# Kernel tuning notes

Hardware: AMD Instinct MI355X
Metric: run time of the kernel (lower is better)

The kernel has to match this reference:

```python
import jax, jax.numpy as jnp
import numpy as np

DIM = 768
H = 12          # num_heads
KV = 4          # kv_heads
D = DIM // H    # head_dim = 64
ROPE_BASE = 10000.0
WINDOW = 8
B, N = 4, 1024


def setup_inputs() -> dict:
    key = jax.random.key(0)
    ks = jax.random.split(key, 8)
    s = 0.02  # weight scale for sane magnitudes
    return {
        "x": jax.random.normal(ks[0], (B, N, DIM), jnp.float32),
        "Wq": jax.random.normal(ks[1], (2 * DIM, DIM), jnp.float32) * s,
        "Wk": jax.random.normal(ks[2], (2 * DIM * KV // H, DIM), jnp.float32) * s,
        "Wv1": jax.random.normal(ks[3], (DIM * KV // H, DIM), jnp.float32) * s,
        "Wv2": jax.random.normal(ks[4], (DIM * KV // H, DIM), jnp.float32) * s,
        "lambda_p": jnp.full((H, 1, 1), -2.0, jnp.float32),
        "Wo": jax.random.normal(ks[5], (DIM, DIM), jnp.float32) * s,
        "bo": jax.random.normal(ks[6], (DIM,), jnp.float32) * s,
    }


def _rotate_half(x):
    x1 = x[..., ::2]
    x2 = x[..., 1::2]
    return jnp.stack([-x2, x1], axis=-1).reshape(x.shape)


def _rope_cos_sin(n, dtype):
    side = int(n ** 0.5)
    if side * side == n:
        h = np.arange(side, dtype=np.float32)
        gh, gw = np.meshgrid(h, h, indexing="ij")
        pos_h, pos_w = gh.reshape(-1), gw.reshape(-1)
    else:
        pos_h = np.arange(n, dtype=np.float32)
        pos_w = np.zeros_like(pos_h)
    dim_half = D // 2
    inv_freq = ROPE_BASE ** (-np.arange(dim_half, dtype=np.float32) / dim_half)
    theta = np.concatenate([pos_h[:, None] * inv_freq[None, :],
                            pos_w[:, None] * inv_freq[None, :]], axis=1)  # [N, D]
    cos = jnp.asarray(np.cos(theta), dtype)[None, None]  # [1,1,N,D]
    sin = jnp.asarray(np.sin(theta), dtype)[None, None]
    return cos, sin


def _apply_rope(q, cos, sin):
    return q * cos + _rotate_half(q) * sin


def _qk_norm(t):
    return t / (jnp.linalg.norm(t, axis=-1, keepdims=True) + 1e-6)


def _window_mask(n, dtype):
    side = int(n ** 0.5)
    if side * side == n:
        h = np.arange(side)
        gh, gw = np.meshgrid(h, h, indexing="ij")
        coords = np.stack([gh.reshape(-1), gw.reshape(-1)], axis=1)  # [N,2]
        dist = np.abs(coords[:, None, :] - coords[None, :, :]).max(-1)  # Chebyshev
    else:
        idx = np.arange(n)
        dist = np.abs(idx[None, :] - idx[:, None])
    return jnp.asarray(np.where(dist > WINDOW, -np.inf, 0.0).astype(np.float32), dtype)


def _attend(q, k, v, mask):
    # q,k,v: [B,H,N,D]; mask additive [N,N]
    scale = 1.0 / np.sqrt(D)
    scores = jnp.einsum("bhnd,bhmd->bhnm", q, k) * scale + mask
    return jnp.einsum("bhnm,bhmd->bhnd", jax.nn.softmax(scores, axis=-1), v)


def reference(x, Wq, Wk, Wv1, Wv2, lambda_p, Wo, bo):
    b, n, c = x.shape
    rep = H // KV
    q = (x @ Wq.T).reshape(b, n, 2, H, D).transpose(2, 0, 3, 1, 4)   # [2,B,H,N,D]
    k = (x @ Wk.T).reshape(b, n, 2, KV, D).transpose(2, 0, 3, 1, 4)  # [2,B,KV,N,D]
    v1 = (x @ Wv1.T).reshape(b, n, KV, D).transpose(0, 2, 1, 3)      # [B,KV,N,D]
    v2 = (x @ Wv2.T).reshape(b, n, KV, D).transpose(0, 2, 1, 3)
    q1, q2 = q[0], q[1]
    k1, k2 = k[0], k[1]
    # GQA: repeat_interleave over head axis
    k1 = jnp.repeat(k1, rep, axis=1)
    k2 = jnp.repeat(k2, rep, axis=1)
    v1 = jnp.repeat(v1, rep, axis=1)
    v2 = jnp.repeat(v2, rep, axis=1)
    cos, sin = _rope_cos_sin(n, x.dtype)
    q1, q2 = _apply_rope(q1, cos, sin), _apply_rope(q2, cos, sin)
    k1, k2 = _apply_rope(k1, cos, sin), _apply_rope(k2, cos, sin)
    q1, q2, k1, k2 = _qk_norm(q1), _qk_norm(q2), _qk_norm(k1), _qk_norm(k2)
    mask = _window_mask(n, x.dtype)
    out1 = _attend(q1, k1, v1, mask)
    out2 = _attend(q2, k2, v2, mask)
    lam = jax.nn.softplus(lambda_p)  # [H,1,1] broadcasts over [B,H,N,D]
    out = out1 - lam[None] * out2
    out = out.transpose(0, 2, 1, 3).reshape(b, n, c)
    return out @ Wo.T + bo
```

## Files before the change

### kernel.cpp

```cpp
#include <hip/hip_runtime.h>
#include <hip/hip_bf16.h>

#define BATCH 4
#define NSEQ  1024
#define DIM   768
#define NH    12
#define NKV   4
#define HD    64
#define NTOK  (BATCH*NSEQ)

using bf16 = __hip_bfloat16;
typedef __attribute__((ext_vector_type(8))) short short8;
typedef __attribute__((ext_vector_type(4))) float floatx4;

__device__ __forceinline__ float b2f(short x) {
  unsigned u = ((unsigned)(unsigned short)x) << 16;
  return __builtin_bit_cast(float, u);
}
__device__ __forceinline__ unsigned short f2b(float f) {
  unsigned u = __builtin_bit_cast(unsigned, f);
  unsigned r = u + 0x7FFF + ((u >> 16) & 1);
  return (unsigned short)(r >> 16);
}

__device__ __forceinline__ void load_lds_16(const bf16* g, bf16* l) {
  __builtin_amdgcn_global_load_lds(
      (const __attribute__((address_space(1))) void*)g,
      (__attribute__((address_space(3))) void*)l, 16, 0, 0);
}

__global__ __launch_bounds__(256) void cvt_all(
    const float* __restrict__ x,  const float* __restrict__ wq,
    const float* __restrict__ wk, const float* __restrict__ wv1,
    const float* __restrict__ wv2, const float* __restrict__ wo,
    bf16* __restrict__ xb,  bf16* __restrict__ wqb, bf16* __restrict__ wkb,
    bf16* __restrict__ wv1b, bf16* __restrict__ wv2b, bf16* __restrict__ wob)
{
  int i = blockIdx.x * 256 + threadIdx.x;
  const float* s; bf16* d; int off;
  if      (i <  786432) { s = x;   d = xb;   off = i; }
  else if (i < 1081344) { s = wq;  d = wqb;  off = i -  786432; }
  else if (i < 1179648) { s = wk;  d = wkb;  off = i - 1081344; }
  else if (i < 1228800) { s = wv1; d = wv1b; off = i - 1179648; }
  else if (i < 1277952) { s = wv2; d = wv2b; off = i - 1228800; }
  else                  { s = wo;  d = wob;  off = i - 1277952; }
  float4 f = reinterpret_cast<const float4*>(s)[off];
  ushort4 u;
  u.x = f2b(f.x); u.y = f2b(f.y); u.z = f2b(f.z); u.w = f2b(f.w);
  reinterpret_cast<ushort4*>(d)[off] = u;
}

__global__ __launch_bounds__(256, 2) void gemm_qkv(
    const bf16* __restrict__ xb,
    const bf16* __restrict__ Wqb, const bf16* __restrict__ Wkb,
    const bf16* __restrict__ Wv1b, const bf16* __restrict__ Wv2b,
    bf16* __restrict__ qb, bf16* __restrict__ kb,
    bf16* __restrict__ v1b, bf16* __restrict__ v2b)
{
  __shared__ __align__(16) bf16 As[128 * 32];
  __shared__ __align__(16) bf16 Ws[128 * 32];

  const int bn = blockIdx.x, bm = blockIdx.y;
  const bf16* Wp; bf16* Yp; int ldY; bool dorope;
  if (bn < 12)      { Wp = Wqb  + (size_t)bn * 128 * 768;        Yp = qb  + bn * 128;        ldY = 1536; dorope = true; }
  else if (bn < 16) { Wp = Wkb  + (size_t)(bn - 12) * 128 * 768; Yp = kb  + (bn - 12) * 128; ldY = 512;  dorope = true; }
  else if (bn < 18) { Wp = Wv1b + (size_t)(bn - 16) * 128 * 768; Yp = v1b + (bn - 16) * 128; ldY = 256;  dorope = false; }
  else              { Wp = Wv2b + (size_t)(bn - 18) * 128 * 768; Yp = v2b + (bn - 18) * 128; ldY = 256;  dorope = false; }

  const int t = threadIdx.x, wave = t >> 6, lane = t & 63;
  const int wm = wave >> 1, wn = wave & 1;
  const int quad = lane >> 4, lr = lane & 15;

  const int srow = wave * 32 + (lane >> 2);
  const int scol = (lane & 3) * 8;
  const bf16* Ag = xb + (size_t)(bm * 128 + srow) * 768 + scol;
  const bf16* Wg = Wp + (size_t)srow * 768 + scol;
  bf16* Al0 = As + wave * 1024;
  bf16* Al1 = As + wave * 1024 + 512;
  bf16* Wl0 = Ws + wave * 1024;
  bf16* Wl1 = Ws + wave * 1024 + 512;

  floatx4 acc[4][4] = {};

  for (int k0 = 0; k0 < 768; k0 += 32) {
    load_lds_16(Ag + k0,            Al0);
    load_lds_16(Ag + 16 * 768 + k0, Al1);
    load_lds_16(Wg + k0,            Wl0);
    load_lds_16(Wg + 16 * 768 + k0, Wl1);
    __syncthreads();

    short8 af[4], wf[4];
    #pragma unroll
    for (int mt = 0; mt < 4; ++mt)
      af[mt] = *reinterpret_cast<const short8*>(&As[(wm * 64 + mt * 16 + lr) * 32 + quad * 8]);
    #pragma unroll
    for (int nt = 0; nt < 4; ++nt)
      wf[nt] = *reinterpret_cast<const short8*>(&Ws[(wn * 64 + nt * 16 + lr) * 32 + quad * 8]);

    #pragma unroll
    for (int mt = 0; mt < 4; ++mt)
      #pragma unroll
      for (int nt = 0; nt < 4; ++nt)
        acc[mt][nt] = __builtin_amdgcn_mfma_f32_16x16x32_bf16(af[mt], wf[nt], acc[mt][nt], 0, 0, 0);
    __syncthreads();
  }

  if (dorope) {
    const float K2 = 0.41524101186098309f;
    const float invf0 = exp2f(-(float)lr * K2);
    const float invf1 = exp2f(-(float)(16 + lr) * K2);
    const float sgn = (lr & 1) ? 1.f : -1.f;
    #pragma unroll
    for (int mt = 0; mt < 4; ++mt) {
      #pragma unroll
      for (int r = 0; r < 4; ++r) {
        int row = bm * 128 + wm * 64 + mt * 16 + quad * 4 + r;
        int n = row & (NSEQ - 1);
        float ph = (float)(n >> 5), pw = (float)(n & 31);
        float v0 = acc[mt][0][r];
        float v1 = acc[mt][1][r];
        float v2 = acc[mt][2][r];
        float v3 = acc[mt][3][r];
        float rot0 = sgn * __shfl_xor(v0, 1);
        float rot1 = sgn * __shfl_xor(v1, 1);
        float rot2 = sgn * __shfl_xor(v2, 1);
        float rot3 = sgn * __shfl_xor(v3, 1);
        float t0 = ph * invf0, t1 = ph * invf1, t2 = pw * invf0, t3 = pw * invf1;
        float rv0 = v0 * __cosf(t0) + rot0 * __sinf(t0);
        float rv1 = v1 * __cosf(t1) + rot1 * __sinf(t1);
        float rv2 = v2 * __cosf(t2) + rot2 * __sinf(t2);
        float rv3 = v3 * __cosf(t3) + rot3 * __sinf(t3);
        float ss = rv0 * rv0 + rv1 * rv1 + rv2 * rv2 + rv3 * rv3;
        #pragma unroll
        for (int off = 1; off < 16; off <<= 1) ss += __shfl_xor(ss, off);
        float sc = 1.f / (sqrtf(ss) + 1e-6f);
        size_t rbase = (size_t)row * ldY + wn * 64 + lr;
        *(unsigned short*)&Yp[rbase +  0] = f2b(rv0 * sc);
        *(unsigned short*)&Yp[rbase + 16] = f2b(rv1 * sc);
        *(unsigned short*)&Yp[rbase + 32] = f2b(rv2 * sc);
        *(unsigned short*)&Yp[rbase + 48] = f2b(rv3 * sc);
      }
    }
  } else {
    #pragma unroll
    for (int mt = 0; mt < 4; ++mt)
      #pragma unroll
      for (int nt = 0; nt < 4; ++nt)
        #pragma unroll
        for (int r = 0; r < 4; ++r) {
          int row = bm * 128 + wm * 64 + mt * 16 + quad * 4 + r;
          int col = wn * 64 + nt * 16 + lr;
          *(unsigned short*)&Yp[(size_t)row * ldY + col] = f2b(acc[mt][nt][r]);
        }
  }
}

__global__ __launch_bounds__(256, 2) void gemm_out(
    const bf16* __restrict__ Xb, const bf16* __restrict__ Wob,
    float* __restrict__ out, const float* __restrict__ bias)
{
  __shared__ __align__(16) bf16 As[128 * 32];
  __shared__ __align__(16) bf16 Ws[128 * 32];

  const int bn = blockIdx.x, bm = blockIdx.y;
  const int t = threadIdx.x, wave = t >> 6, lane = t & 63;
  const int wm = wave >> 1, wn = wave & 1;
  const int quad = lane >> 4, lr = lane & 15;

  const int srow = wave * 32 + (lane >> 2);
  const int scol = (lane & 3) * 8;
  const bf16* Ag = Xb  + (size_t)(bm * 128 + srow) * 768 + scol;
  const bf16* Wg = Wob + (size_t)(bn * 128 + srow) * 768 + scol;
  bf16* Al0 = As + wave * 1024;
  bf16* Al1 = As + wave * 1024 + 512;
  bf16* Wl0 = Ws + wave * 1024;
  bf16* Wl1 = Ws + wave * 1024 + 512;

  floatx4 acc[4][4] = {};

  for (int k0 = 0; k0 < 768; k0 += 32) {
    load_lds_16(Ag + k0,            Al0);
    load_lds_16(Ag + 16 * 768 + k0, Al1);
    load_lds_16(Wg + k0,            Wl0);
    load_lds_16(Wg + 16 * 768 + k0, Wl1);
    __syncthreads();

    short8 af[4], wf[4];
    #pragma unroll
    for (int mt = 0; mt < 4; ++mt)
      af[mt] = *reinterpret_cast<const short8*>(&As[(wm * 64 + mt * 16 + lr) * 32 + quad * 8]);
    #pragma unroll
    for (int nt = 0; nt < 4; ++nt)
      wf[nt] = *reinterpret_cast<const short8*>(&Ws[(wn * 64 + nt * 16 + lr) * 32 + quad * 8]);

    #pragma unroll
    for (int mt = 0; mt < 4; ++mt)
      #pragma unroll
      for (int nt = 0; nt < 4; ++nt)
        acc[mt][nt] = __builtin_amdgcn_mfma_f32_16x16x32_bf16(af[mt], wf[nt], acc[mt][nt], 0, 0, 0);
    __syncthreads();
  }

  #pragma unroll
  for (int nt = 0; nt < 4; ++nt) {
    int col = bn * 128 + wn * 64 + nt * 16 + lr;
    float bv = bias[col];
    #pragma unroll
    for (int mt = 0; mt < 4; ++mt)
      #pragma unroll
      for (int r = 0; r < 4; ++r) {
        int row = bm * 128 + wm * 64 + mt * 16 + quad * 4 + r;
        out[(size_t)row * 768 + col] = acc[mt][nt][r] + bv;
      }
  }
}

__global__ __launch_bounds__(256) void repack_kv(
    const bf16* __restrict__ kb,
    const bf16* __restrict__ v1b, const bf16* __restrict__ v2b,
    bf16* __restrict__ Kpk, bf16* __restrict__ Vpk1, bf16* __restrict__ Vpk2)
{
  int blk = blockIdx.x;
  int t = threadIdx.x;
  if (blk < 1024) {
    int kh = blk & 31;
    int kvh = (blk >> 5) & 3;
    int sb = blk >> 7;
    int s = sb & 1, b = sb >> 1;
    int nt = t >> 7, ks = (t >> 6) & 1, quad = (t >> 4) & 3, lr = t & 15;
    const bf16* src = kb + (size_t)(b * 1024 + kh * 32 + nt * 16 + lr) * 512
                         + s * 256 + kvh * 64 + ks * 32 + quad * 8;
    short8 v = *reinterpret_cast<const short8*>(src);
    *reinterpret_cast<short8*>(Kpk + (size_t)blk * 2048 + t * 8) = v;
  } else {
    int id = blk - 1024;
    int s = id >> 9;
    int rem = id & 511;
    int kh = rem & 31;
    int kvh = (rem >> 5) & 3;
    int b = rem >> 7;
    const bf16* vsrc = s ? v2b : v1b;
    bf16* vdst = s ? Vpk2 : Vpk1;
    int quad = (t >> 4) & 3, lr = t & 15;
    const bf16* base = vsrc + (size_t)(b * 1024 + kh * 32 + quad * 8) * 256
                            + kvh * 64 + (t >> 6) * 16 + lr;
    short8 o;
    #pragma unroll
    for (int j = 0; j < 8; ++j) o[j] = *(const short*)(base + j * 256);
    *reinterpret_cast<short8*>(vdst + (size_t)rem * 2048 + t * 8) = o;
  }
}

struct Frag { short8 kf[2][2]; short8 vf[4]; };

__device__ __forceinline__ void attn_load(
    Frag& f, const bf16* __restrict__ kp, const bf16* __restrict__ vp,
    int kh, int lane8)
{
  const bf16* kt = kp + (size_t)kh * 2048 + lane8;
  const bf16* vt = vp + (size_t)kh * 2048 + lane8;
  f.kf[0][0] = *reinterpret_cast<const short8*>(kt);
  f.kf[0][1] = *reinterpret_cast<const short8*>(kt + 512);
  f.kf[1][0] = *reinterpret_cast<const short8*>(kt + 1024);
  f.kf[1][1] = *reinterpret_cast<const short8*>(kt + 1536);
  f.vf[0] = *reinterpret_cast<const short8*>(vt);
  f.vf[1] = *reinterpret_cast<const short8*>(vt + 512);
  f.vf[2] = *reinterpret_cast<const short8*>(vt + 1024);
  f.vf[3] = *reinterpret_cast<const short8*>(vt + 1536);
}

__device__ __forceinline__ void attn_step(
    const short8 (&qf)[2][2], const Frag& f, unsigned maskbits,
    floatx4 (&O)[2][4], float (&psum)[2][4], bf16* __restrict__ Pl,
    int quad, int lr)
{
  floatx4 S[2][2] = {};
  #pragma unroll
  for (int ks = 0; ks < 2; ++ks) {
    S[0][0] = __builtin_amdgcn_mfma_f32_16x16x32_bf16(qf[0][ks], f.kf[0][ks], S[0][0], 0, 0, 0);
    S[0][1] = __builtin_amdgcn_mfma_f32_16x16x32_bf16(qf[0][ks], f.kf[1][ks], S[0][1], 0, 0, 0);
    S[1][0] = __builtin_amdgcn_mfma_f32_16x16x32_bf16(qf[1][ks], f.kf[0][ks], S[1][0], 0, 0, 0);
    S[1][1] = __builtin_amdgcn_mfma_f32_16x16x32_bf16(qf[1][ks], f.kf[1][ks], S[1][1], 0, 0, 0);
  }

  #pragma unroll
  for (int mt = 0; mt < 2; ++mt)
    #pragma unroll
    for (int nt = 0; nt < 2; ++nt)
      #pragma unroll
      for (int r = 0; r < 4; ++r) {
        float p = __expf(S[mt][nt][r] * 0.125f);
        p = ((maskbits >> (mt * 8 + nt * 4 + r)) & 1u) ? p : 0.0f;
        psum[mt][r] += p;
        *(unsigned short*)&Pl[(mt * 16 + quad * 4 + r) * 40 + nt * 16 + lr] = f2b(p);
      }

  short8 pf0 = *reinterpret_cast<const short8*>(&Pl[(lr) * 40 + quad * 8]);
  short8 pf1 = *reinterpret_cast<const short8*>(&Pl[(16 + lr) * 40 + quad * 8]);
  #pragma unroll
  for (int ntd = 0; ntd < 4; ++ntd) {
    O[0][ntd] = __builtin_amdgcn_mfma_f32_16x16x32_bf16(pf0, f.vf[ntd], O[0][ntd], 0, 0, 0);
    O[1][ntd] = __builtin_amdgcn_mfma_f32_16x16x32_bf16(pf1, f.vf[ntd], O[1][ntd], 0, 0, 0);
  }
}

__global__ __launch_bounds__(256, 2) void attn_mfma(
    const bf16* __restrict__ q, const bf16* __restrict__ Kpk,
    const bf16* __restrict__ Vpk1, const bf16* __restrict__ Vpk2,
    const float* __restrict__ lambda_p, bf16* __restrict__ X)
{
  __shared__ __align__(16) char smem[25088];

  const int bid = blockIdx.x;
  const int qh = bid & 31;
  const int hb = bid >> 5;
  const int h  = hb % 12;
  const int b  = hb / 12;
  const int kvh = h / 3;

  const int t = threadIdx.x;
  const int w = t >> 6;
  const int s = w >> 1;
  const int half = w & 1;
  const int lane = t & 63;
  const int quad = lane >> 4, lr = lane & 15;
  const int lane8 = lane * 8;

  bf16* Pl = (bf16*)(smem + w * 2560);
  float* Oslab = (float*)(smem + s * 8192);
  float* Pslab = (float*)(smem + 16384 + s * 2048);
  bf16* Xs = (bf16*)(smem + 20480);

  const int tok0 = b * NSEQ + qh * 32;

  short8 qf[2][2];
  #pragma unroll
  for (int mt = 0; mt < 2; ++mt)
    #pragma unroll
    for (int ks = 0; ks < 2; ++ks)
      qf[mt][ks] = *reinterpret_cast<const short8*>(
          q + (size_t)(tok0 + mt * 16 + lr) * 1536 + s * 768 + h * 64 + ks * 32 + quad * 8);

  unsigned maskbits = 0;
  #pragma unroll
  for (int mt = 0; mt < 2; ++mt)
    #pragma unroll
    for (int nt = 0; nt < 2; ++nt)
      #pragma unroll
      for (int r = 0; r < 4; ++r) {
        int qq = mt * 16 + quad * 4 + r;
        int km = nt * 16 + lr;
        int d = km - qq; if (d < 0) d = -d;
        if (d <= 8) maskbits |= 1u << (mt * 8 + nt * 4 + r);
      }

  floatx4 O[2][4] = {};
  float psum[2][4] = {};

  const int kh0 = (qh > 8) ? qh - 8 : 0;
  const int kh1 = (qh < 23) ? qh + 8 : 31;
  const int cnt = kh1 - kh0 + 1;
  const int cA = (cnt + 1) >> 1;
  const int khA = half ? kh0 + cA : kh0;
  const int khB = half ? kh1 : kh0 + cA - 1;

  const bf16* kpbase = Kpk + (size_t)((b * 2 + s) * 4 + kvh) * 32 * 2048;
  const bf16* vpbase = (s ? Vpk2 : Vpk1) + (size_t)(b * 4 + kvh) * 32 * 2048;

  Frag fA, fB;
  attn_load(fA, kpbase, vpbase, khA, lane8);
  attn_load(fB, kpbase, vpbase, (khA + 1 <= khB) ? khA + 1 : khB, lane8);

  int i = khA;
  while (true) {
    attn_step(qf, fA, maskbits, O, psum, Pl, quad, lr);
    if (i == khB) break;
    ++i;
    attn_load(fA, kpbase, vpbase, (i + 1 <= khB) ? i + 1 : i, lane8);
    attn_step(qf, fB, maskbits, O, psum, Pl, quad, lr);
    if (i == khB) break;
    ++i;
    attn_load(fB, kpbase, vpbase, (i + 1 <= khB) ? i + 1 : i, lane8);
  }

  __syncthreads();
  if (half == 1) {
    #pragma unroll
    for (int mt = 0; mt < 2; ++mt)
      #pragma unroll
      for (int ntd = 0; ntd < 4; ++ntd)
        *reinterpret_cast<floatx4*>(&Oslab[(mt * 4 + ntd) * 256 + lane * 4]) = O[mt][ntd];
    floatx4 p0, p1;
    p0[0] = psum[0][0]; p0[1] = psum[0][1]; p0[2] = psum[0][2]; p0[3] = psum[0][3];
    p1[0] = psum[1][0]; p1[1] = psum[1][1]; p1[2] = psum[1][2]; p1[3] = psum[1][3];
    *reinterpret_cast<floatx4*>(&Pslab[lane * 4])       = p0;
    *reinterpret_cast<floatx4*>(&Pslab[256 + lane * 4]) = p1;
  }
  __syncthreads();
  if (half == 0) {
    #pragma unroll
    for (int mt = 0; mt < 2; ++mt)
      #pragma unroll
      for (int ntd = 0; ntd < 4; ++ntd)
        O[mt][ntd] += *reinterpret_cast<const floatx4*>(&Oslab[(mt * 4 + ntd) * 256 + lane * 4]);
    floatx4 p0 = *reinterpret_cast<const floatx4*>(&Pslab[lane * 4]);
    floatx4 p1 = *reinterpret_cast<const floatx4*>(&Pslab[256 + lane * 4]);
    #pragma unroll
    for (int r = 0; r < 4; ++r) { psum[0][r] += p0[r]; psum[1][r] += p1[r]; }

    #pragma unroll
    for (int off = 1; off < 16; off <<= 1)
      #pragma unroll
      for (int mt = 0; mt < 2; ++mt)
        #pragma unroll
        for (int r = 0; r < 4; ++r)
          psum[mt][r] += __shfl_xor(psum[mt][r], off);
    #pragma unroll
    for (int mt = 0; mt < 2; ++mt)
      #pragma unroll
      for (int r = 0; r < 4; ++r)
        psum[mt][r] = 1.f / psum[mt][r];
    #pragma unroll
    for (int mt = 0; mt < 2; ++mt)
      #pragma unroll
      for (int ntd = 0; ntd < 4; ++ntd)
        #pragma unroll
        for (int r = 0; r < 4; ++r)
          O[mt][ntd][r] *= psum[mt][r];

    if (s == 1) {
      #pragma unroll
      for (int mt = 0; mt < 2; ++mt)
        #pragma unroll
        for (int ntd = 0; ntd < 4; ++ntd)
          *reinterpret_cast<floatx4*>(&Oslab[(mt * 4 + ntd) * 256 + lane * 4]) = O[mt][ntd];
    }
  }
  __syncthreads();
  if (w == 0) {
    float lam = log1pf(__expf(lambda_p[h]));
    const float* O2slab = (const float*)(smem + 8192);
    #pragma unroll
    for (int mt = 0; mt < 2; ++mt)
      #pragma unroll
      for (int ntd = 0; ntd < 4; ++ntd) {
        floatx4 o2 = *reinterpret_cast<const floatx4*>(&O2slab[(mt * 4 + ntd) * 256 + lane * 4]);
        #pragma unroll
        for (int r = 0; r < 4; ++r) {
          float xv = O[mt][ntd][r] - lam * o2[r];
          *(unsigned short*)&Xs[(mt * 16 + quad * 4 + r) * 72 + ntd * 16 + lr] = f2b(xv);
        }
      }
  }
  __syncthreads();

  {
    int row = t >> 3, seg = t & 7;
    short8 xv = *reinterpret_cast<const short8*>(&Xs[row * 72 + seg * 8]);
    *reinterpret_cast<short8*>(X + (size_t)(tok0 + row) * 768 + h * 64 + seg * 8) = xv;
  }
}

extern "C" void kernel_launch(void* const* d_in, const int* in_sizes, int n_in,
                              void* d_out, int out_size, void* d_ws, size_t ws_size,
                              hipStream_t stream)
{
  const float* x        = (const float*)d_in[0];
  const float* Wq       = (const float*)d_in[1];
  const float* Wk       = (const float*)d_in[2];
  const float* Wv1      = (const float*)d_in[3];
  const float* Wv2      = (const float*)d_in[4];
  const float* lambda_p = (const float*)d_in[5];
  const float* Wo       = (const float*)d_in[6];
  const float* bo       = (const float*)d_in[7];
  float* out = (float*)d_out;

  bf16* xb   = (bf16*)d_ws;
  bf16* Wqb  = xb   + (size_t)NTOK * 768;
  bf16* Wkb  = Wqb  + (size_t)1536 * 768;
  bf16* Wv1b = Wkb  + (size_t)512 * 768;
  bf16* Wv2b = Wv1b + (size_t)256 * 768;
  bf16* Wob  = Wv2b + (size_t)256 * 768;
  bf16* qb   = Wob  + (size_t)768 * 768;
  bf16* kb   = qb   + (size_t)NTOK * 1536;
  bf16* v1b  = kb   + (size_t)NTOK * 512;
  bf16* v2b  = v1b  + (size_t)NTOK * 256;
  bf16* Xb   = v2b  + (size_t)NTOK * 256;
  bf16* Vpk1 = Xb   + (size_t)NTOK * 768;
  bf16* Vpk2 = Vpk1 + (size_t)512 * 2048;
  bf16* Kpk  = Vpk2 + (size_t)512 * 2048;

  cvt_all<<<5568, 256, 0, stream>>>(x, Wq, Wk, Wv1, Wv2, Wo,
                                    xb, Wqb, Wkb, Wv1b, Wv2b, Wob);

  gemm_qkv<<<dim3(20, 32), 256, 0, stream>>>(xb, Wqb, Wkb, Wv1b, Wv2b,
                                             qb, kb, v1b, v2b);

  repack_kv<<<2048, 256, 0, stream>>>(kb, v1b, v2b, Kpk, Vpk1, Vpk2);

  attn_mfma<<<BATCH * NH * 32, 256, 0, stream>>>(qb, Kpk, Vpk1, Vpk2, lambda_p, Xb);

  gemm_out<<<dim3(6, 32), 256, 0, stream>>>(Xb, Wob, out, bo);
}
```

Before: 163.6 us.

## Fuse KV repack into QKV GEMM epilogue and split attention across four waves per stream

The QKV GEMM epilogue now writes K and V straight into the packed layouts the attention kernel reads, so the separate repack_kv launch and its global round trip go away. The attention kernel moves from 256 to 512 threads, with four waves per stream each handling a quarter of the key-block range instead of two halves. Partial outputs and row sums are merged through a two-stage LDS reduction. This adds scattered 2-byte stores in the GEMM epilogue, more LDS and more barriers in attention, and may lower occupancy.

```diff
diff --git a/kernel.cpp b/kernel.cpp
--- a/kernel.cpp
+++ b/kernel.cpp
@@ -54,18 +54,18 @@
     const bf16* __restrict__ xb,
     const bf16* __restrict__ Wqb, const bf16* __restrict__ Wkb,
     const bf16* __restrict__ Wv1b, const bf16* __restrict__ Wv2b,
-    bf16* __restrict__ qb, bf16* __restrict__ kb,
-    bf16* __restrict__ v1b, bf16* __restrict__ v2b)
+    bf16* __restrict__ qb, bf16* __restrict__ Kpk,
+    bf16* __restrict__ Vpk1, bf16* __restrict__ Vpk2)
 {
   __shared__ __align__(16) bf16 As[128 * 32];
   __shared__ __align__(16) bf16 Ws[128 * 32];
 
   const int bn = blockIdx.x, bm = blockIdx.y;
-  const bf16* Wp; bf16* Yp; int ldY; bool dorope;
-  if (bn < 12)      { Wp = Wqb  + (size_t)bn * 128 * 768;        Yp = qb  + bn * 128;        ldY = 1536; dorope = true; }
-  else if (bn < 16) { Wp = Wkb  + (size_t)(bn - 12) * 128 * 768; Yp = kb  + (bn - 12) * 128; ldY = 512;  dorope = true; }
-  else if (bn < 18) { Wp = Wv1b + (size_t)(bn - 16) * 128 * 768; Yp = v1b + (bn - 16) * 128; ldY = 256;  dorope = false; }
-  else              { Wp = Wv2b + (size_t)(bn - 18) * 128 * 768; Yp = v2b + (bn - 18) * 128; ldY = 256;  dorope = false; }
+  const bf16* Wp;
+  if (bn < 12)      Wp = Wqb  + (size_t)bn * 128 * 768;
+  else if (bn < 16) Wp = Wkb  + (size_t)(bn - 12) * 128 * 768;
+  else if (bn < 18) Wp = Wv1b + (size_t)(bn - 16) * 128 * 768;
+  else              Wp = Wv2b + (size_t)(bn - 18) * 128 * 768;
 
   const int t = threadIdx.x, wave = t >> 6, lane = t & 63;
   const int wm = wave >> 1, wn = wave & 1;
@@ -105,11 +105,15 @@
     __syncthreads();
   }
 
-  if (dorope) {
+  if (bn < 16) {
     const float K2 = 0.41524101186098309f;
     const float invf0 = exp2f(-(float)lr * K2);
     const float invf1 = exp2f(-(float)(16 + lr) * K2);
     const float sgn = (lr & 1) ? 1.f : -1.f;
+    const bool isq = (bn < 12);
+    const int hh = (bn - 12) * 2 + wn;
+    const int s_ = hh >> 2, kvh_ = hh & 3;
+    const int qk128 = (lr >> 3) * 128;
     #pragma unroll
     for (int mt = 0; mt < 4; ++mt) {
       #pragma unroll
@@ -134,24 +138,43 @@
         #pragma unroll
         for (int off = 1; off < 16; off <<= 1) ss += __shfl_xor(ss, off);
         float sc = 1.f / (sqrtf(ss) + 1e-6f);
-        size_t rbase = (size_t)row * ldY + wn * 64 + lr;
-        *(unsigned short*)&Yp[rbase +  0] = f2b(rv0 * sc);
-        *(unsigned short*)&Yp[rbase + 16] = f2b(rv1 * sc);
-        *(unsigned short*)&Yp[rbase + 32] = f2b(rv2 * sc);
-        *(unsigned short*)&Yp[rbase + 48] = f2b(rv3 * sc);
+        if (isq) {
+          size_t rbase = (size_t)row * 1536 + bn * 128 + wn * 64 + lr;
+          *(unsigned short*)&qb[rbase +  0] = f2b(rv0 * sc);
+          *(unsigned short*)&qb[rbase + 16] = f2b(rv1 * sc);
+          *(unsigned short*)&qb[rbase + 32] = f2b(rv2 * sc);
+          *(unsigned short*)&qb[rbase + 48] = f2b(rv3 * sc);
+        } else {
+          int bb = row >> 10, kh = n >> 5;
+          bf16* tb = Kpk + ((size_t)((bb * 2 + s_) * 4 + kvh_) * 32 + kh) * 2048
+                     + (mt & 1) * 1024 + (quad * 4 + r) * 8 + (lr & 7) + qk128;
+          *(unsigned short*)&tb[0]   = f2b(rv0 * sc);
+          *(unsigned short*)&tb[256] = f2b(rv1 * sc);
+          *(unsigned short*)&tb[512] = f2b(rv2 * sc);
+          *(unsigned short*)&tb[768] = f2b(rv3 * sc);
+        }
       }
     }
   } else {
-    #pragma unroll
-    for (int mt = 0; mt < 4; ++mt)
-      #pragma unroll
-      for (int nt = 0; nt < 4; ++nt)
-        #pragma unroll
-        for (int r = 0; r < 4; ++r) {
-          int row = bm * 128 + wm * 64 + mt * 16 + quad * 4 + r;
-          int col = wn * 64 + nt * 16 + lr;
-          *(unsigned short*)&Yp[(size_t)row * ldY + col] = f2b(acc[mt][nt][r]);
-        }
+    const bool is2 = (bn >= 18);
+    bf16* Vp = is2 ? Vpk2 : Vpk1;
+    const int kvh_ = (bn - (is2 ? 18 : 16)) * 2 + wn;
+    #pragma unroll
+    for (int mt = 0; mt < 4; ++mt)
+      #pragma unroll
+      for (int r = 0; r < 4; ++r) {
+        int row = bm * 128 + wm * 64 + mt * 16 + quad * 4 + r;
+        int n = row & (NSEQ - 1);
+        int bb = row >> 10, kh = n >> 5;
+        int rowm = (mt & 1) * 16 + quad * 4 + r;
+        int quad_v = rowm >> 3, j = rowm & 7;
+        bf16* tb = Vp + ((size_t)(bb * 4 + kvh_) * 32 + kh) * 2048
+                   + quad_v * 128 + lr * 8 + j;
+        *(unsigned short*)&tb[0]    = f2b(acc[mt][0][r]);
+        *(unsigned short*)&tb[512]  = f2b(acc[mt][1][r]);
+        *(unsigned short*)&tb[1024] = f2b(acc[mt][2][r]);
+        *(unsigned short*)&tb[1536] = f2b(acc[mt][3][r]);
+      }
   }
 }
 
@@ -212,42 +235,6 @@
         int row = bm * 128 + wm * 64 + mt * 16 + quad * 4 + r;
         out[(size_t)row * 768 + col] = acc[mt][nt][r] + bv;
       }
-  }
-}
-
-__global__ __launch_bounds__(256) void repack_kv(
-    const bf16* __restrict__ kb,
-    const bf16* __restrict__ v1b, const bf16* __restrict__ v2b,
-    bf16* __restrict__ Kpk, bf16* __restrict__ Vpk1, bf16* __restrict__ Vpk2)
-{
-  int blk = blockIdx.x;
-  int t = threadIdx.x;
-  if (blk < 1024) {
-    int kh = blk & 31;
-    int kvh = (blk >> 5) & 3;
-    int sb = blk >> 7;
-    int s = sb & 1, b = sb >> 1;
-    int nt = t >> 7, ks = (t >> 6) & 1, quad = (t >> 4) & 3, lr = t & 15;
-    const bf16* src = kb + (size_t)(b * 1024 + kh * 32 + nt * 16 + lr) * 512
-                         + s * 256 + kvh * 64 + ks * 32 + quad * 8;
-    short8 v = *reinterpret_cast<const short8*>(src);
-    *reinterpret_cast<short8*>(Kpk + (size_t)blk * 2048 + t * 8) = v;
-  } else {
-    int id = blk - 1024;
-    int s = id >> 9;
-    int rem = id & 511;
-    int kh = rem & 31;
-    int kvh = (rem >> 5) & 3;
-    int b = rem >> 7;
-    const bf16* vsrc = s ? v2b : v1b;
-    bf16* vdst = s ? Vpk2 : Vpk1;
-    int quad = (t >> 4) & 3, lr = t & 15;
-    const bf16* base = vsrc + (size_t)(b * 1024 + kh * 32 + quad * 8) * 256
-                            + kvh * 64 + (t >> 6) * 16 + lr;
-    short8 o;
-    #pragma unroll
-    for (int j = 0; j < 8; ++j) o[j] = *(const short*)(base + j * 256);
-    *reinterpret_cast<short8*>(vdst + (size_t)rem * 2048 + t * 8) = o;
   }
 }
 
@@ -304,12 +291,12 @@
   }
 }
 
-__global__ __launch_bounds__(256, 2) void attn_mfma(
+__global__ __launch_bounds__(512, 2) void attn_mfma(
     const bf16* __restrict__ q, const bf16* __restrict__ Kpk,
     const bf16* __restrict__ Vpk1, const bf16* __restrict__ Vpk2,
     const float* __restrict__ lambda_p, bf16* __restrict__ X)
 {
-  __shared__ __align__(16) char smem[25088];
+  __shared__ __align__(16) char smem[40960];
 
   const int bid = blockIdx.x;
   const int qh = bid & 31;
@@ -320,16 +307,13 @@
 
   const int t = threadIdx.x;
   const int w = t >> 6;
-  const int s = w >> 1;
-  const int half = w & 1;
+  const int s = w >> 2;
+  const int qtr = w & 3;
   const int lane = t & 63;
   const int quad = lane >> 4, lr = lane & 15;
   const int lane8 = lane * 8;
 
   bf16* Pl = (bf16*)(smem + w * 2560);
-  float* Oslab = (float*)(smem + s * 8192);
-  float* Pslab = (float*)(smem + 16384 + s * 2048);
-  bf16* Xs = (bf16*)(smem + 20480);
 
   const int tok0 = b * NSEQ + qh * 32;
 
@@ -360,54 +344,61 @@
   const int kh0 = (qh > 8) ? qh - 8 : 0;
   const int kh1 = (qh < 23) ? qh + 8 : 31;
   const int cnt = kh1 - kh0 + 1;
-  const int cA = (cnt + 1) >> 1;
-  const int khA = half ? kh0 + cA : kh0;
-  const int khB = half ? kh1 : kh0 + cA - 1;
+  const int st = kh0 + (cnt * qtr) / 4;
+  const int en = kh0 + (cnt * (qtr + 1)) / 4 - 1;
 
   const bf16* kpbase = Kpk + (size_t)((b * 2 + s) * 4 + kvh) * 32 * 2048;
   const bf16* vpbase = (s ? Vpk2 : Vpk1) + (size_t)(b * 4 + kvh) * 32 * 2048;
 
   Frag fA, fB;
-  attn_load(fA, kpbase, vpbase, khA, lane8);
-  attn_load(fB, kpbase, vpbase, (khA + 1 <= khB) ? khA + 1 : khB, lane8);
-
-  int i = khA;
+  attn_load(fA, kpbase, vpbase, st, lane8);
+  attn_load(fB, kpbase, vpbase, (st + 1 <= en) ? st + 1 : en, lane8);
+
+  int i = st;
   while (true) {
     attn_step(qf, fA, maskbits, O, psum, Pl, quad, lr);
-    if (i == khB) break;
+    if (i == en) break;
     ++i;
-    attn_load(fA, kpbase, vpbase, (i + 1 <= khB) ? i + 1 : i, lane8);
+    attn_load(fA, kpbase, vpbase, (i + 1 <= en) ? i + 1 : i, lane8);
     attn_step(qf, fB, maskbits, O, psum, Pl, quad, lr);
-    if (i == khB) break;
+    if (i == en) break;
     ++i;
-    attn_load(fB, kpbase, vpbase, (i + 1 <= khB) ? i + 1 : i, lane8);
-  }
-
-  __syncthreads();
-  if (half == 1) {
+    attn_load(fB, kpbase, vpbase, (i + 1 <= en) ? i + 1 : i, lane8);
+  }
+
+  auto writeslab = [&](float* sl) {
     #pragma unroll
     for (int mt = 0; mt < 2; ++mt)
       #pragma unroll
       for (int ntd = 0; ntd < 4; ++ntd)
-        *reinterpret_cast<floatx4*>(&Oslab[(mt * 4 + ntd) * 256 + lane * 4]) = O[mt][ntd];
+        *reinterpret_cast<floatx4*>(&sl[(mt * 4 + ntd) * 256 + lane * 4]) = O[mt][ntd];
     floatx4 p0, p1;
     p0[0] = psum[0][0]; p0[1] = psum[0][1]; p0[2] = psum[0][2]; p0[3] = psum[0][3];
     p1[0] = psum[1][0]; p1[1] = psum[1][1]; p1[2] = psum[1][2]; p1[3] = psum[1][3];
-    *reinterpret_cast<floatx4*>(&Pslab[lane * 4])       = p0;
-    *reinterpret_cast<floatx4*>(&Pslab[256 + lane * 4]) = p1;
-  }
-  __syncthreads();
-  if (half == 0) {
+    *reinterpret_cast<floatx4*>(&sl[2048 + lane * 4])       = p0;
+    *reinterpret_cast<floatx4*>(&sl[2048 + 256 + lane * 4]) = p1;
+  };
+  auto readaddslab = [&](const float* sl) {
     #pragma unroll
     for (int mt = 0; mt < 2; ++mt)
       #pragma unroll
       for (int ntd = 0; ntd < 4; ++ntd)
-        O[mt][ntd] += *reinterpret_cast<const floatx4*>(&Oslab[(mt * 4 + ntd) * 256 + lane * 4]);
-    floatx4 p0 = *reinterpret_cast<const floatx4*>(&Pslab[lane * 4]);
-    floatx4 p1 = *reinterpret_cast<const floatx4*>(&Pslab[256 + lane * 4]);
+        O[mt][ntd] += *reinterpret_cast<const floatx4*>(&sl[(mt * 4 + ntd) * 256 + lane * 4]);
+    floatx4 p0 = *reinterpret_cast<const floatx4*>(&sl[2048 + lane * 4]);
+    floatx4 p1 = *reinterpret_cast<const floatx4*>(&sl[2048 + 256 + lane * 4]);
     #pragma unroll
     for (int r = 0; r < 4; ++r) { psum[0][r] += p0[r]; psum[1][r] += p1[r]; }
-
+  };
+
+  __syncthreads();
+  if (qtr & 1) writeslab((float*)(smem + (s * 2 + (qtr >> 1)) * 10240));
+  __syncthreads();
+  if (!(qtr & 1)) readaddslab((const float*)(smem + (s * 2 + (qtr >> 1)) * 10240));
+  __syncthreads();
+  if (qtr == 2) writeslab((float*)(smem + (s * 2 + 1) * 10240));
+  __syncthreads();
+  if (qtr == 0) {
+    readaddslab((const float*)(smem + (s * 2 + 1) * 10240));
     #pragma unroll
     for (int off = 1; off < 16; off <<= 1)
       #pragma unroll
@@ -427,24 +418,25 @@
         #pragma unroll
         for (int r = 0; r < 4; ++r)
           O[mt][ntd][r] *= psum[mt][r];
-
     if (s == 1) {
+      float* sl = (float*)(smem + 2 * 10240);
       #pragma unroll
       for (int mt = 0; mt < 2; ++mt)
         #pragma unroll
         for (int ntd = 0; ntd < 4; ++ntd)
-          *reinterpret_cast<floatx4*>(&Oslab[(mt * 4 + ntd) * 256 + lane * 4]) = O[mt][ntd];
+          *reinterpret_cast<floatx4*>(&sl[(mt * 4 + ntd) * 256 + lane * 4]) = O[mt][ntd];
     }
   }
   __syncthreads();
+  bf16* Xs = (bf16*)(smem + 10240);
   if (w == 0) {
     float lam = log1pf(__expf(lambda_p[h]));
-    const float* O2slab = (const float*)(smem + 8192);
+    const float* sl = (const float*)(smem + 2 * 10240);
     #pragma unroll
     for (int mt = 0; mt < 2; ++mt)
       #pragma unroll
       for (int ntd = 0; ntd < 4; ++ntd) {
-        floatx4 o2 = *reinterpret_cast<const floatx4*>(&O2slab[(mt * 4 + ntd) * 256 + lane * 4]);
+        floatx4 o2 = *reinterpret_cast<const floatx4*>(&sl[(mt * 4 + ntd) * 256 + lane * 4]);
         #pragma unroll
         for (int r = 0; r < 4; ++r) {
           float xv = O[mt][ntd][r] - lam * o2[r];
@@ -454,7 +446,7 @@
   }
   __syncthreads();
 
-  {
+  if (t < 256) {
     int row = t >> 3, seg = t & 7;
     short8 xv = *reinterpret_cast<const short8*>(&Xs[row * 72 + seg * 8]);
     *reinterpret_cast<short8*>(X + (size_t)(tok0 + row) * 768 + h * 64 + seg * 8) = xv;
@@ -482,10 +474,7 @@
   bf16* Wv2b = Wv1b + (size_t)256 * 768;
   bf16* Wob  = Wv2b + (size_t)256 * 768;
   bf16* qb   = Wob  + (size_t)768 * 768;
-  bf16* kb   = qb   + (size_t)NTOK * 1536;
-  bf16* v1b  = kb   + (size_t)NTOK * 512;
-  bf16* v2b  = v1b  + (size_t)NTOK * 256;
-  bf16* Xb   = v2b  + (size_t)NTOK * 256;
+  bf16* Xb   = qb   + (size_t)NTOK * 1536;
   bf16* Vpk1 = Xb   + (size_t)NTOK * 768;
   bf16* Vpk2 = Vpk1 + (size_t)512 * 2048;
   bf16* Kpk  = Vpk2 + (size_t)512 * 2048;
@@ -494,11 +483,9 @@
                                     xb, Wqb, Wkb, Wv1b, Wv2b, Wob);
 
   gemm_qkv<<<dim3(20, 32), 256, 0, stream>>>(xb, Wqb, Wkb, Wv1b, Wv2b,
-                                             qb, kb, v1b, v2b);
-
-  repack_kv<<<2048, 256, 0, stream>>>(kb, v1b, v2b, Kpk, Vpk1, Vpk2);
-
-  attn_mfma<<<BATCH * NH * 32, 256, 0, stream>>>(qb, Kpk, Vpk1, Vpk2, lambda_p, Xb);
+                                             qb, Kpk, Vpk1, Vpk2);
+
+  attn_mfma<<<BATCH * NH * 32, 512, 0, stream>>>(qb, Kpk, Vpk1, Vpk2, lambda_p, Xb);
 
   gemm_out<<<dim3(6, 32), 256, 0, stream>>>(Xb, Wob, out, bo);
 }
```

Result: slower. 187.0 us (+14.3%).
